# Kernel optimization log

Hardware: AMD Instinct MI355X
Metric: run time of the kernel (lower is better)

Reference implementation:

```python
import math
import jax, jax.numpy as jnp
import numpy as np

NUM_HEADS = 16
D_MODEL = 1024
WINDOW = 512


def alibi_slopes(num_heads):
    # 1 / ((2**8)**((i+1)/num_heads))  for i in range(num_heads)
    x = (2.0 ** 8) ** (1.0 / num_heads)
    return jnp.asarray([1.0 / x ** (i + 1) for i in range(num_heads)], dtype=jnp.float32)


def setup_inputs() -> dict:
    key = jax.random.key(0)
    k1, k2 = jax.random.split(key)
    x = jax.random.normal(k1, (1, 4096, D_MODEL), dtype=jnp.float32)
    # scale weight like a trained init so softmax isn't saturated
    w_kqv = jax.random.normal(k2, (D_MODEL, 3 * D_MODEL), dtype=jnp.float32) * 0.02
    return {"x": x, "w_kqv": w_kqv}


def reference(x, w_kqv):
    B, S, D = x.shape
    H = NUM_HEADS
    hd = D // H
    scale = math.sqrt(D)  # module scales by sqrt(d_model), not sqrt(head_dim)

    kqv = x @ w_kqv                       # [B, S, 3D]
    k, q, v = jnp.split(kqv, 3, axis=-1)  # chunk order: key, query, value
    k = k.reshape(B, S, H, hd).transpose(0, 2, 1, 3)  # [B, H, S, hd]
    q = q.reshape(B, S, H, hd).transpose(0, 2, 1, 3)
    v = v.reshape(B, S, H, hd).transpose(0, 2, 1, 3)

    # ALiBi bias: m_h * (j - i)
    pos = jnp.arange(S)
    rel = pos[None, :] - pos[:, None]                  # [S, S] = x - y
    bias = alibi_slopes(H)[:, None, None] * rel.astype(jnp.float32)  # [H, S, S]

    score = jnp.einsum("bhqd,bhkd->bhqk", q, k) / scale + bias[None]

    # causal sliding-window mask: allow 0 <= i - j <= WINDOW
    dist = pos[:, None] - pos[None, :]                 # i - j
    mask = (dist >= 0) & (dist <= WINDOW)              # [S, S]
    score = jnp.where(mask[None, None], score, -jnp.inf)

    attn = jax.nn.softmax(score, axis=-1)
    out = jnp.einsum("bhqk,bhkd->bhqd", attn, v)       # [B, H, S, hd]
    out = out.transpose(0, 2, 1, 3).reshape(B, S, D)
    return out
```

## Files before the change

### kernel.cpp

```cpp
#include <hip/hip_runtime.h>
#include <hip/hip_bf16.h>

#define SEQ   4096
#define DM    1024
#define NH    16
#define HD    64
#define N3    3072
#define WIN   512

#define LOG2E 1.4426950408889634f

typedef __attribute__((ext_vector_type(8))) short short8;
typedef __attribute__((ext_vector_type(4))) short short4v;
typedef __attribute__((ext_vector_type(4))) float float4v;

__device__ __forceinline__ float bf16_bits_to_float(unsigned short u) {
  return __uint_as_float(((unsigned int)u) << 16);
}

typedef __attribute__((address_space(3))) void lds_void_t;
typedef __attribute__((address_space(1))) const void gbl_void_t;
__device__ __forceinline__ void async_copy16(void* lds_dst, const void* g_src) {
  __builtin_amdgcn_global_load_lds((gbl_void_t*)g_src, (lds_void_t*)lds_dst,
                                   16, 0, 0);
}

template <int NT>
__device__ __forceinline__ int detect_fp32(const unsigned short* __restrict__ probe,
                                           float* red) {
  const int t = threadIdx.x;
  float mx = 0.0f;
#pragma unroll
  for (int p = 0; p < 8; ++p) {
    float v = bf16_bits_to_float(probe[(t * 8 + p) * 2]);
    if (v != v) v = 1e38f;
    mx = fmaxf(mx, fabsf(v));
  }
  red[t] = mx;
  __syncthreads();
  for (int s = NT / 2; s > 0; s >>= 1) {
    if (t < s) red[t] = fmaxf(red[t], red[t + s]);
    __syncthreads();
  }
  const int fl = red[0] > 100.0f ? 1 : 0;
  __syncthreads();
  return fl;
}

__device__ __forceinline__ int detect_fp32_wave(
    const unsigned short* __restrict__ probe) {
  const int lane = threadIdx.x & 63;
  float mx = 0.0f;
#pragma unroll
  for (int p = 0; p < 8; ++p) {
    float v = bf16_bits_to_float(probe[(lane * 8 + p) * 2]);
    if (v != v) v = 1e38f;
    mx = fmaxf(mx, fabsf(v));
  }
  return __any(mx > 100.0f) ? 1 : 0;
}

__global__ __launch_bounds__(256) void prep(
    const void* __restrict__ x, const void* __restrict__ w,
    __hip_bfloat16* __restrict__ xb, __hip_bfloat16* __restrict__ wt) {
  __shared__ __hip_bfloat16 tile[64][66];
  __shared__ float red[256];
  const int t = threadIdx.x;
  if (blockIdx.x < 2048) {
    const int fl = detect_fp32<256>((const unsigned short*)x, red);
    const int i0 = (blockIdx.x * 256 + t) * 8;
    if (fl) {
      const float* xf = (const float*)x + i0;
      float4 f0 = *(const float4*)(xf);
      float4 f1 = *(const float4*)(xf + 4);
      __hip_bfloat16 tmp[8];
      tmp[0] = __float2bfloat16(f0.x); tmp[1] = __float2bfloat16(f0.y);
      tmp[2] = __float2bfloat16(f0.z); tmp[3] = __float2bfloat16(f0.w);
      tmp[4] = __float2bfloat16(f1.x); tmp[5] = __float2bfloat16(f1.y);
      tmp[6] = __float2bfloat16(f1.z); tmp[7] = __float2bfloat16(f1.w);
      *(uint4*)&xb[i0] = *(const uint4*)tmp;
    } else {
      *(uint4*)&xb[i0] = *(const uint4*)((const __hip_bfloat16*)x + i0);
    }
  } else {
    const int bid = blockIdx.x - 2048;
    const int fl = detect_fp32<256>((const unsigned short*)w, red);
    const int n0 = (bid % 48) * 64;
    const int k0 = (bid / 48) * 64;
    const int tx = t & 63, ty0 = t >> 6;
    if (fl) {
      const float* wf = (const float*)w;
#pragma unroll
      for (int p = 0; p < 16; ++p) {
        int row = ty0 + p * 4;
        tile[row][tx] = __float2bfloat16(wf[(k0 + row) * N3 + n0 + tx]);
      }
    } else {
      const __hip_bfloat16* wb = (const __hip_bfloat16*)w;
#pragma unroll
      for (int p = 0; p < 16; ++p) {
        int row = ty0 + p * 4;
        tile[row][tx] = wb[(k0 + row) * N3 + n0 + tx];
      }
    }
    __syncthreads();
#pragma unroll
    for (int r = 0; r < 2; ++r) {
      int oe = r * 2048 + t * 8;
      int nr = oe >> 6, kc = oe & 63;
      __hip_bfloat16 v[8];
#pragma unroll
      for (int e = 0; e < 8; ++e) v[e] = tile[kc + e][nr];
      *(uint4*)&wt[(n0 + nr) * DM + k0 + kc] = *(const uint4*)v;
    }
  }
}

__global__ __launch_bounds__(512, 2) void gemm_kqv(
    const __hip_bfloat16* __restrict__ A,
    const __hip_bfloat16* __restrict__ BT,
    __hip_bfloat16* __restrict__ C) {
  __shared__ __align__(16) __hip_bfloat16 As[2][2][128 * 32];
  __shared__ __align__(16) __hip_bfloat16 Bs[2][192 * 64];

  const int flat = blockIdx.y * 16 + blockIdx.x;
  const int swz  = (flat & 7) * 64 + (flat >> 3);
  const int m0 = (swz >> 4) * 128;
  const int n0 = (swz & 15) * 192;

  const int t = threadIdx.x;
  const int wave = t >> 6, lane = t & 63;
  const int wm = wave >> 2, wn = wave & 3;
  const int l15 = lane & 15, quad = lane >> 4;

  const int arow = t >> 2;
  const int acol = ((t & 3) ^ (arow & 3)) * 8;
  const long aoff = (long)(m0 + arow) * DM + acol;
  const int brow = t >> 3;
  const int bcol = ((t & 7) ^ (brow & 7)) * 8;
  const long boff0 = (long)(n0 +       brow) * DM + bcol;
  const long boff1 = (long)(n0 +  64 + brow) * DM + bcol;
  const long boff2 = (long)(n0 + 128 + brow) * DM + bcol;
  const int ldst = t * 16;

#define STAGE_B(buf, kt) do { \
    const int ko_ = (kt) * 64; \
    async_copy16((char*)Bs[buf]         + ldst, &BT[boff0 + ko_]); \
    async_copy16((char*)Bs[buf] +  8192 + ldst, &BT[boff1 + ko_]); \
    async_copy16((char*)Bs[buf] + 16384 + ldst, &BT[boff2 + ko_]); } while (0)
#define STAGE_A(buf, kt) do { \
    const int ko_ = (kt) * 64; \
    async_copy16((char*)As[buf][0] + ldst, &A[aoff + ko_]); \
    async_copy16((char*)As[buf][1] + ldst, &A[aoff + ko_ + 32]); } while (0)

  float4v acc[4][3] = {};

  STAGE_B(0, 0); STAGE_A(0, 0);
  asm volatile("s_waitcnt vmcnt(0)" ::: "memory");
  __builtin_amdgcn_s_barrier();

  for (int kt = 0; kt < 16; ++kt) {
    const int P = kt & 1, N = P ^ 1;
    short8 a[4], b[3];

#pragma unroll
    for (int h = 0; h < 2; ++h) {
      const char* Ap = (const char*)As[P][h];
      const char* Bp = (const char*)Bs[P];
#pragma unroll
      for (int mi = 0; mi < 4; ++mi) {
        const int row = wm * 64 + mi * 16 + l15;
        a[mi] = *(const short8*)(Ap + row * 64 + ((quad ^ (row & 3)) << 4));
      }
#pragma unroll
      for (int ni = 0; ni < 3; ++ni) {
        const int row = wn * 48 + ni * 16 + l15;
        b[ni] = *(const short8*)(Bp + row * 128 +
                                 ((((h << 2) + quad) ^ (row & 7)) << 4));
      }
      if (h == 0) {
        if (kt < 15) {
          STAGE_B(N, kt + 1);
          asm volatile("s_waitcnt vmcnt(3)" ::: "memory");
        } else {
          asm volatile("s_waitcnt vmcnt(0)" ::: "memory");
        }
      } else {
        if (kt < 15) STAGE_A(N, kt + 1);
        asm volatile("s_waitcnt vmcnt(1)" ::: "memory");
      }
      __builtin_amdgcn_s_barrier();
      __builtin_amdgcn_s_setprio(1);
#pragma unroll
      for (int mi = 0; mi < 4; ++mi)
#pragma unroll
        for (int ni = 0; ni < 3; ++ni)
          acc[mi][ni] = __builtin_amdgcn_mfma_f32_16x16x32_bf16(
              a[mi], b[ni], acc[mi][ni], 0, 0, 0);
      __builtin_amdgcn_s_setprio(0);
      __builtin_amdgcn_s_barrier();
    }
  }
#undef STAGE_A
#undef STAGE_B

#pragma unroll
  for (int mi = 0; mi < 4; ++mi)
#pragma unroll
    for (int ni = 0; ni < 3; ++ni)
#pragma unroll
      for (int r = 0; r < 4; ++r) {
        int row = m0 + wm * 64 + mi * 16 + quad * 4 + r;
        int col = n0 + wn * 48 + ni * 16 + l15;
        C[row * N3 + col] = __float2bfloat16(acc[mi][ni][r]);
      }
}

__global__ __launch_bounds__(256, 4) void attn(
    const __hip_bfloat16* __restrict__ kqv,
    const unsigned short* __restrict__ xprobe,
    void* __restrict__ out) {
  __shared__ __align__(16) __hip_bfloat16 Ks[64 * 72];
  __shared__ __align__(16) __hip_bfloat16 Vt[80 * 72];
  __shared__ __align__(16) __hip_bfloat16 Ps[64 * 72];

  const int fl = detect_fp32_wave(xprobe);
  const int h  = blockIdx.y;
  const int bx = blockIdx.x;
  const int i0 = 64 * ((bx & 7) * 8 + (bx >> 3));
  const int t    = threadIdx.x;
  const int wave = t >> 6, lane = t & 63;
  const int l15 = lane & 15, quad = lane >> 4;
  const float slope2  = exp2f(-0.5f * (float)(h + 1)) * LOG2E;
  const float nslope2 = -slope2;
  const float qscale  = LOG2E / 32.0f;

  for (int idx = t; idx < 16 * 64; idx += 256) {
    int rr = idx >> 6, cc = idx & 63;
    ((unsigned short*)Vt)[(64 + rr) * 72 + cc] = (rr == 0) ? 0x3F80 : 0;
  }

  short8 aq[2];
#pragma unroll
  for (int ks2 = 0; ks2 < 2; ++ks2)
    aq[ks2] = *(const short8*)&kqv[(i0 + wave * 16 + l15) * N3 + DM + h * HD +
                                   ks2 * 32 + quad * 8];

  float4v o[5] = {};

  const int jlo  = max(0, i0 - WIN);
  const int nblk = (i0 + 64 - jlo) >> 6;

  const int krow0 = t >> 3, krow1 = (t >> 3) + 32, kd0 = (t & 7) * 8;
  const int rbase = t >> 3;
  const int vd0   = (t & 7) * 8;
  const int kA    = (rbase & 15) + ((rbase >> 4) << 5);
  const int vsig2 = (((rbase & 15) << 2) + ((rbase >> 4) << 1)) * 2;
  const int vswz  = (t & 7) << 4;
  uint4 kregA, kregB, vregA, vregB;
  kregA = *(const uint4*)&kqv[(jlo + krow0) * N3 + h * HD + kd0];
  kregB = *(const uint4*)&kqv[(jlo + krow1) * N3 + h * HD + kd0];
  vregA = *(const uint4*)&kqv[(jlo + kA) * N3 + 2 * DM + h * HD + vd0];
  vregB = *(const uint4*)&kqv[(jlo + kA + 16) * N3 + 2 * DM + h * HD + vd0];

  for (int b = 0; b < nblk; ++b) {
    const int j0 = jlo + b * 64;
    __syncthreads();
    *(uint4*)&Ks[krow0 * 72 + kd0] = kregA;
    *(uint4*)&Ks[krow1 * 72 + kd0] = kregB;
    {
      const unsigned short* pa = (const unsigned short*)&vregA;
      const unsigned short* pb = (const unsigned short*)&vregB;
      char* vbase = (char*)Vt;
#pragma unroll
      for (int e = 0; e < 8; ++e) {
        unsigned int pack = (unsigned int)pa[e] | ((unsigned int)pb[e] << 16);
        *(unsigned int*)(vbase + (vd0 + e) * 144 + (vsig2 ^ vswz)) = pack;
      }
    }
    __syncthreads();

    if (b + 1 < nblk) {
      const int jn = j0 + 64;
      kregA = *(const uint4*)&kqv[(jn + krow0) * N3 + h * HD + kd0];
      kregB = *(const uint4*)&kqv[(jn + krow1) * N3 + h * HD + kd0];
      vregA = *(const uint4*)&kqv[(jn + kA) * N3 + 2 * DM + h * HD + vd0];
      vregB = *(const uint4*)&kqv[(jn + kA + 16) * N3 + 2 * DM + h * HD + vd0];
    }

    float4v sacc[4] = {};
#pragma unroll
    for (int ks2 = 0; ks2 < 2; ++ks2)
#pragma unroll
      for (int nt = 0; nt < 4; ++nt) {
        short8 bk = *(const short8*)&Ks[(nt * 16 + l15) * 72 + ks2 * 32 + quad * 8];
        sacc[nt] = __builtin_amdgcn_mfma_f32_16x16x32_bf16(aq[ks2], bk, sacc[nt], 0, 0, 0);
      }

    const int dbase = (i0 + wave * 16 + quad * 4) - (j0 + l15);
    const float s16 = nslope2 * -16.0f;
    const int psbase = (wave * 16 + quad * 4) * 72 + l15 * 4;
#pragma unroll
    for (int r = 0; r < 4; ++r) {
      float bias = nslope2 * (float)(dbase + r);
      int rel = dbase + r;
      short4v pk;
#pragma unroll
      for (int nt = 0; nt < 4; ++nt) {
        float x = fmaf(sacc[nt][r], qscale, bias);
        x = ((unsigned)rel <= (unsigned)WIN) ? x : -200.0f;
        __hip_bfloat16 hb = __float2bfloat16(exp2f(x));
        pk[nt] = *reinterpret_cast<const short*>(&hb);
        bias += s16;
        rel -= 16;
      }
      *(short4v*)&Ps[psbase + r * 72] = pk;
    }

#pragma unroll
    for (int ks = 0; ks < 64; ks += 32) {
      short8 ap = *(const short8*)&Ps[(wave * 16 + l15) * 72 + ks + quad * 8];
#pragma unroll
      for (int dt = 0; dt < 5; ++dt) {
        const int vrow = dt * 16 + l15;
        const short8 bv = *(const short8*)((const char*)Vt + vrow * 144 +
            ((ks * 2 + (quad << 4)) ^ (((vrow >> 3) & 7) << 4)));
        o[dt] = __builtin_amdgcn_mfma_f32_16x16x32_bf16(ap, bv, o[dt], 0, 0, 0);
      }
    }
  }

#pragma unroll
  for (int r = 0; r < 4; ++r) {
    const float l = __shfl(o[4][r], quad * 16, 64);
    const float inv_l = 1.0f / l;
    const int row = i0 + wave * 16 + quad * 4 + r;
#pragma unroll
    for (int dt = 0; dt < 4; ++dt) {
      const int idx = row * DM + h * HD + dt * 16 + l15;
      const float v = o[dt][r] * inv_l;
      if (fl) ((float*)out)[idx] = v;
      else    ((__hip_bfloat16*)out)[idx] = __float2bfloat16(v);
    }
  }
}

extern "C" void kernel_launch(void* const* d_in, const int* in_sizes, int n_in,
                              void* d_out, int out_size, void* d_ws, size_t ws_size,
                              hipStream_t stream) {
  char* ws = (char*)d_ws;
  __hip_bfloat16* wt  = (__hip_bfloat16*)(ws + 4096);
  __hip_bfloat16* kqv = (__hip_bfloat16*)(ws + 4096 + 6291456);
  __hip_bfloat16* xb  = (__hip_bfloat16*)d_out;

  hipLaunchKernelGGL(prep, dim3(2048 + 768), dim3(256), 0, stream,
                     d_in[0], d_in[1], xb, wt);
  hipLaunchKernelGGL(gemm_kqv, dim3(16, 32), dim3(512), 0, stream, xb, wt, kqv);
  hipLaunchKernelGGL(attn, dim3(64, 16), dim3(256), 0, stream,
                     kqv, (const unsigned short*)d_in[0], d_out);
}
```

Baseline: 141.7 us.

## Double-buffer K/V tiles in LDS, swizzle layouts, compute row sums in registers

K and V tiles are now double-buffered in LDS, so the next tile is written during the current block's compute and only one barrier per block remains instead of two. Padded strides of 72 are replaced with unpadded 64-wide rows using an XOR swizzle to avoid bank conflicts. The fifth MFMA column that used a ones-row in V to get softmax denominators is removed. Row sums are instead accumulated from the bf16-rounded probabilities and reduced across lanes with shuffles at the end. This uses more LDS, which may lower occupancy, and adds some VALU work for the sums.

Measured after the change: 143.0 us. About the same (+0.9%).

```diff
diff --git a/kernel.cpp b/kernel.cpp
--- a/kernel.cpp
+++ b/kernel.cpp
@@ -216,13 +216,15 @@
       }
 }
 
+#define SWZ(row) (((((row) ^ ((row) >> 3))) & 7) << 4)
+
 __global__ __launch_bounds__(256, 4) void attn(
     const __hip_bfloat16* __restrict__ kqv,
     const unsigned short* __restrict__ xprobe,
     void* __restrict__ out) {
-  __shared__ __align__(16) __hip_bfloat16 Ks[64 * 72];
-  __shared__ __align__(16) __hip_bfloat16 Vt[80 * 72];
-  __shared__ __align__(16) __hip_bfloat16 Ps[64 * 72];
+  __shared__ __align__(16) __hip_bfloat16 Ks[2][64 * 64];
+  __shared__ __align__(16) __hip_bfloat16 Vt[2][64 * 64];
+  __shared__ __align__(16) __hip_bfloat16 Ps[64 * 64];
 
   const int fl = detect_fp32_wave(xprobe);
   const int h  = blockIdx.y;
@@ -231,14 +233,8 @@
   const int t    = threadIdx.x;
   const int wave = t >> 6, lane = t & 63;
   const int l15 = lane & 15, quad = lane >> 4;
-  const float slope2  = exp2f(-0.5f * (float)(h + 1)) * LOG2E;
-  const float nslope2 = -slope2;
+  const float nslope2 = -exp2f(-0.5f * (float)(h + 1)) * LOG2E;
   const float qscale  = LOG2E / 32.0f;
-
-  for (int idx = t; idx < 16 * 64; idx += 256) {
-    int rr = idx >> 6, cc = idx & 63;
-    ((unsigned short*)Vt)[(64 + rr) * 72 + cc] = (rr == 0) ? 0x3F80 : 0;
-  }
 
   short8 aq[2];
 #pragma unroll
@@ -246,94 +242,128 @@
     aq[ks2] = *(const short8*)&kqv[(i0 + wave * 16 + l15) * N3 + DM + h * HD +
                                    ks2 * 32 + quad * 8];
 
-  float4v o[5] = {};
+  float4v o[4] = {};
+  float lsum[4] = {0.f, 0.f, 0.f, 0.f};
 
   const int jlo  = max(0, i0 - WIN);
   const int nblk = (i0 + 64 - jlo) >> 6;
 
   const int krow0 = t >> 3, krow1 = (t >> 3) + 32, kd0 = (t & 7) * 8;
+  const int kdst0 = krow0 * 128 + ((kd0 * 2) ^ SWZ(krow0));
+  const int kdst1 = krow1 * 128 + ((kd0 * 2) ^ SWZ(krow1));
   const int rbase = t >> 3;
   const int vd0   = (t & 7) * 8;
   const int kA    = (rbase & 15) + ((rbase >> 4) << 5);
-  const int vsig2 = (((rbase & 15) << 2) + ((rbase >> 4) << 1)) * 2;
-  const int vswz  = (t & 7) << 4;
+  const int vsig2 = ((rbase & 15) * 8) + ((rbase >> 4) * 4);
+
   uint4 kregA, kregB, vregA, vregB;
   kregA = *(const uint4*)&kqv[(jlo + krow0) * N3 + h * HD + kd0];
   kregB = *(const uint4*)&kqv[(jlo + krow1) * N3 + h * HD + kd0];
   vregA = *(const uint4*)&kqv[(jlo + kA) * N3 + 2 * DM + h * HD + vd0];
   vregB = *(const uint4*)&kqv[(jlo + kA + 16) * N3 + 2 * DM + h * HD + vd0];
 
+  {
+    *(uint4*)((char*)Ks[0] + kdst0) = kregA;
+    *(uint4*)((char*)Ks[0] + kdst1) = kregB;
+    const unsigned short* pa = (const unsigned short*)&vregA;
+    const unsigned short* pb = (const unsigned short*)&vregB;
+#pragma unroll
+    for (int e = 0; e < 8; ++e) {
+      unsigned int pack = (unsigned int)pa[e] | ((unsigned int)pb[e] << 16);
+      *(unsigned int*)((char*)Vt[0] + (vd0 + e) * 128 + (vsig2 ^ SWZ(vd0 + e))) = pack;
+    }
+  }
+  if (nblk > 1) {
+    const int jn = jlo + 64;
+    kregA = *(const uint4*)&kqv[(jn + krow0) * N3 + h * HD + kd0];
+    kregB = *(const uint4*)&kqv[(jn + krow1) * N3 + h * HD + kd0];
+    vregA = *(const uint4*)&kqv[(jn + kA) * N3 + 2 * DM + h * HD + vd0];
+    vregB = *(const uint4*)&kqv[(jn + kA + 16) * N3 + 2 * DM + h * HD + vd0];
+  }
+  __syncthreads();
+
   for (int b = 0; b < nblk; ++b) {
-    const int j0 = jlo + b * 64;
-    __syncthreads();
-    *(uint4*)&Ks[krow0 * 72 + kd0] = kregA;
-    *(uint4*)&Ks[krow1 * 72 + kd0] = kregB;
-    {
-      const unsigned short* pa = (const unsigned short*)&vregA;
-      const unsigned short* pb = (const unsigned short*)&vregB;
-      char* vbase = (char*)Vt;
-#pragma unroll
-      for (int e = 0; e < 8; ++e) {
-        unsigned int pack = (unsigned int)pa[e] | ((unsigned int)pb[e] << 16);
-        *(unsigned int*)(vbase + (vd0 + e) * 144 + (vsig2 ^ vswz)) = pack;
-      }
-    }
-    __syncthreads();
-
-    if (b + 1 < nblk) {
-      const int jn = j0 + 64;
-      kregA = *(const uint4*)&kqv[(jn + krow0) * N3 + h * HD + kd0];
-      kregB = *(const uint4*)&kqv[(jn + krow1) * N3 + h * HD + kd0];
-      vregA = *(const uint4*)&kqv[(jn + kA) * N3 + 2 * DM + h * HD + vd0];
-      vregB = *(const uint4*)&kqv[(jn + kA + 16) * N3 + 2 * DM + h * HD + vd0];
-    }
+    const int cur = b & 1, nxt = cur ^ 1;
 
     float4v sacc[4] = {};
 #pragma unroll
     for (int ks2 = 0; ks2 < 2; ++ks2)
 #pragma unroll
       for (int nt = 0; nt < 4; ++nt) {
-        short8 bk = *(const short8*)&Ks[(nt * 16 + l15) * 72 + ks2 * 32 + quad * 8];
+        const int row = nt * 16 + l15;
+        short8 bk = *(const short8*)((const char*)Ks[cur] + row * 128 +
+                                     ((ks2 * 64 + quad * 16) ^ SWZ(row)));
         sacc[nt] = __builtin_amdgcn_mfma_f32_16x16x32_bf16(aq[ks2], bk, sacc[nt], 0, 0, 0);
       }
 
-    const int dbase = (i0 + wave * 16 + quad * 4) - (j0 + l15);
+    const int dbase = (i0 + wave * 16 + quad * 4) - (jlo + b * 64 + l15);
     const float s16 = nslope2 * -16.0f;
-    const int psbase = (wave * 16 + quad * 4) * 72 + l15 * 4;
 #pragma unroll
     for (int r = 0; r < 4; ++r) {
       float bias = nslope2 * (float)(dbase + r);
       int rel = dbase + r;
       short4v pk;
+      float ls = 0.0f;
 #pragma unroll
       for (int nt = 0; nt < 4; ++nt) {
         float x = fmaf(sacc[nt][r], qscale, bias);
         x = ((unsigned)rel <= (unsigned)WIN) ? x : -200.0f;
         __hip_bfloat16 hb = __float2bfloat16(exp2f(x));
-        pk[nt] = *reinterpret_cast<const short*>(&hb);
+        unsigned short bits = *reinterpret_cast<const unsigned short*>(&hb);
+        pk[nt] = (short)bits;
+        ls += bf16_bits_to_float(bits);
         bias += s16;
         rel -= 16;
       }
-      *(short4v*)&Ps[psbase + r * 72] = pk;
+      lsum[r] += ls;
+      const int prow = wave * 16 + quad * 4 + r;
+      *(short4v*)((char*)Ps + prow * 128 + ((l15 * 8) ^ SWZ(prow))) = pk;
+    }
+
+    if (b + 1 < nblk) {
+      *(uint4*)((char*)Ks[nxt] + kdst0) = kregA;
+      *(uint4*)((char*)Ks[nxt] + kdst1) = kregB;
+      const unsigned short* pa = (const unsigned short*)&vregA;
+      const unsigned short* pb = (const unsigned short*)&vregB;
+#pragma unroll
+      for (int e = 0; e < 8; ++e) {
+        unsigned int pack = (unsigned int)pa[e] | ((unsigned int)pb[e] << 16);
+        *(unsigned int*)((char*)Vt[nxt] + (vd0 + e) * 128 + (vsig2 ^ SWZ(vd0 + e))) = pack;
+      }
+      if (b + 2 < nblk) {
+        const int jn = jlo + (b + 2) * 64;
+        kregA = *(const uint4*)&kqv[(jn + krow0) * N3 + h * HD + kd0];
+        kregB = *(const uint4*)&kqv[(jn + krow1) * N3 + h * HD + kd0];
+        vregA = *(const uint4*)&kqv[(jn + kA) * N3 + 2 * DM + h * HD + vd0];
+        vregB = *(const uint4*)&kqv[(jn + kA + 16) * N3 + 2 * DM + h * HD + vd0];
+      }
     }
 
 #pragma unroll
     for (int ks = 0; ks < 64; ks += 32) {
-      short8 ap = *(const short8*)&Ps[(wave * 16 + l15) * 72 + ks + quad * 8];
-#pragma unroll
-      for (int dt = 0; dt < 5; ++dt) {
+      const int prow = wave * 16 + l15;
+      short8 ap = *(const short8*)((const char*)Ps + prow * 128 +
+                                   ((ks * 2 + quad * 16) ^ SWZ(prow)));
+#pragma unroll
+      for (int dt = 0; dt < 4; ++dt) {
         const int vrow = dt * 16 + l15;
-        const short8 bv = *(const short8*)((const char*)Vt + vrow * 144 +
-            ((ks * 2 + (quad << 4)) ^ (((vrow >> 3) & 7) << 4)));
+        short8 bv = *(const short8*)((const char*)Vt[cur] + vrow * 128 +
+                                     ((ks * 2 + quad * 16) ^ SWZ(vrow)));
         o[dt] = __builtin_amdgcn_mfma_f32_16x16x32_bf16(ap, bv, o[dt], 0, 0, 0);
       }
     }
+
+    __syncthreads();
   }
 
 #pragma unroll
   for (int r = 0; r < 4; ++r) {
-    const float l = __shfl(o[4][r], quad * 16, 64);
-    const float inv_l = 1.0f / l;
+    float s = lsum[r];
+    s += __shfl_xor(s, 1, 64);
+    s += __shfl_xor(s, 2, 64);
+    s += __shfl_xor(s, 4, 64);
+    s += __shfl_xor(s, 8, 64);
+    const float inv_l = 1.0f / s;
     const int row = i0 + wave * 16 + quad * 4 + r;
 #pragma unroll
     for (int dt = 0; dt < 4; ++dt) {
```
